# Kernel tuning notes

Measured on AMD Instinct MI355X. Metric: run time of the kernel, lower is better.

Reference implementation:

```python
import jax, jax.numpy as jnp
import numpy as np

N_MOL = 100000   # molecules in batch
N_ATOMS = 40     # atoms per molecule
R = 2            # resonance representations per molecule


def setup_inputs() -> dict:
    key = jax.random.key(0)
    k1, k2, k3 = jax.random.split(key, 3)
    N = N_MOL * N_ATOMS * R  # flattened atom rows (8M)
    electronegativity = jax.random.normal(k1, (N,), dtype=jnp.float32)
    # hardness must be positive / away from zero (it is inverted)
    hardness = jax.random.uniform(k2, (N,), dtype=jnp.float32, minval=0.5, maxval=1.5)
    formal_charge = jax.random.randint(k3, (N,), -1, 2).astype(jnp.float32)
    idx = jnp.arange(N, dtype=jnp.int32)
    # layout: [mol0 rep0 (40 atoms), mol0 rep1 (40 atoms), mol1 rep0, ...]
    rep_seg = idx // N_ATOMS                       # molecule-representation segment id
    mol = idx // (N_ATOMS * R)
    j = idx % N_ATOMS                              # atom index within molecule
    out_idx = mol * N_ATOMS + j                    # output row for mean over reps
    return {
        "electronegativity": electronegativity,
        "hardness": hardness,
        "formal_charge": formal_charge,
        "rep_seg": rep_seg,
        "out_idx": out_idx,
        "num_segments": N_MOL * R,
        "num_out": N_MOL * N_ATOMS,
        "n_reps": R,
    }


def reference(electronegativity, hardness, formal_charge, rep_seg, out_idx,
              num_segments, num_out, n_reps):
    # Charge equalization (Gilson et al.) per molecule-representation segment s:
    #   inv_h_i = 1/h_i
    #   q_i = inv_h_i * ((dot(inv_h, e) + Q_s) / sum(inv_h) - e_i)
    inv_h = 1.0 / hardness
    A = jax.ops.segment_sum(inv_h, rep_seg, num_segments)                      # sum(1/h)
    B = jax.ops.segment_sum(inv_h * electronegativity, rep_seg, num_segments)  # dot(1/h, e)
    Q = jax.ops.segment_sum(formal_charge, rep_seg, num_segments)              # total charge
    lam = (B + Q) / A                                                          # Lagrange multiplier per segment
    q = inv_h * (lam[rep_seg] - electronegativity)                             # per-atom charge per rep
    # mean over the n_reps representations of each molecule (torch .mean(dim=0) + vstack)
    out = jax.ops.segment_sum(q, out_idx, num_out) / n_reps
    return out.reshape(-1, 1)
```

## Files before the change

### kernel.cpp

```cpp
#include <hip/hip_runtime.h>


#define BLOCK 320
#define MPB   16
#define SEGS  (MPB * 2)
#define ATOMS (MPB * 80)

__global__ __launch_bounds__(BLOCK) void cpc_kernel(
    const float* __restrict__ elneg,
    const float* __restrict__ hard,
    const float* __restrict__ fchg,
    float* __restrict__ out,
    int n_mol)
{
    __shared__ float s_inv[ATOMS];
    __shared__ float s_e[ATOMS];
    __shared__ float s_pa[SEGS * 11];
    __shared__ float s_pb[SEGS * 11];
    __shared__ float s_pq[SEGS * 11];
    __shared__ float s_lam[SEGS];

    const int t = threadIdx.x;
    const long long mol_base = (long long)blockIdx.x * MPB;
    const int lm = (int)min((long long)MPB, (long long)n_mol - mol_base);
    const long long atom_base = mol_base * 80;

    if (t < lm * 20) {
        const int a4 = 4 * t;
        float4 h4 = *reinterpret_cast<const float4*>(hard  + atom_base + a4);
        float4 e4 = *reinterpret_cast<const float4*>(elneg + atom_base + a4);
        float4 f4 = *reinterpret_cast<const float4*>(fchg  + atom_base + a4);
        float4 i4;
        i4.x = 1.0f / h4.x; i4.y = 1.0f / h4.y;
        i4.z = 1.0f / h4.z; i4.w = 1.0f / h4.w;
        *reinterpret_cast<float4*>(&s_inv[a4]) = i4;
        *reinterpret_cast<float4*>(&s_e[a4])   = e4;
        const float pa = (i4.x + i4.y) + (i4.z + i4.w);
        const float pb = (i4.x * e4.x + i4.y * e4.y) + (i4.z * e4.z + i4.w * e4.w);
        const float pq = (f4.x + f4.y) + (f4.z + f4.w);
        const int seg  = t / 10;
        const int slot = t % 10;
        s_pa[seg * 11 + slot] = pa;
        s_pb[seg * 11 + slot] = pb;
        s_pq[seg * 11 + slot] = pq;
    }
    __syncthreads();

    if (t < lm * 2) {
        float A = 0.f, B = 0.f, Q = 0.f;
        #pragma unroll
        for (int k = 0; k < 10; ++k) {
            A += s_pa[t * 11 + k];
            B += s_pb[t * 11 + k];
            Q += s_pq[t * 11 + k];
        }
        s_lam[t] = (B + Q) / A;
    }
    __syncthreads();

    if (t < lm * 10) {
        const int m = t / 10;
        const int j = (t % 10) * 4;
        const float lam0 = s_lam[2 * m];
        const float lam1 = s_lam[2 * m + 1];
        const int p0 = m * 80 + j;
        const int p1 = p0 + 40;
        float4 i0 = *reinterpret_cast<const float4*>(&s_inv[p0]);
        float4 e0 = *reinterpret_cast<const float4*>(&s_e[p0]);
        float4 i1 = *reinterpret_cast<const float4*>(&s_inv[p1]);
        float4 e1 = *reinterpret_cast<const float4*>(&s_e[p1]);
        float4 o;
        o.x = 0.5f * (i0.x * (lam0 - e0.x) + i1.x * (lam1 - e1.x));
        o.y = 0.5f * (i0.y * (lam0 - e0.y) + i1.y * (lam1 - e1.y));
        o.z = 0.5f * (i0.z * (lam0 - e0.z) + i1.z * (lam1 - e1.z));
        o.w = 0.5f * (i0.w * (lam0 - e0.w) + i1.w * (lam1 - e1.w));
        *reinterpret_cast<float4*>(out + mol_base * 40 + 4 * t) = o;
    }
}

extern "C" void kernel_launch(void* const* d_in, const int* in_sizes, int n_in,
                              void* d_out, int out_size, void* d_ws, size_t ws_size,
                              hipStream_t stream) {
    const float* elneg = (const float*)d_in[0];
    const float* hard  = (const float*)d_in[1];
    const float* fchg  = (const float*)d_in[2];
    float* out = (float*)d_out;

    const int n_mol = out_size / 40;
    const int grid  = (n_mol + MPB - 1) / MPB;
    cpc_kernel<<<grid, BLOCK, 0, stream>>>(elneg, hard, fchg, out, n_mol);
}
```

Baseline: 22.17 us.

## Keep atom data in registers, double molecules per block, use nontemporal loads

Each thread now loads both representations of its 4-atom slice, keeps the inverse hardness and electronegativity in registers, and reuses them for the final charge, which removes the shared-memory staging arrays and their stores and reloads. Molecules per block rise from 16 to 32 at 320 threads, so every thread is active and the grid halves. Global loads and stores use nontemporal builtins to avoid polluting the cache with streamed data. Each thread now holds more registers, and the loads of the two representations are strided by 40 floats instead of fully contiguous per thread.

```diff
diff --git a/kernel.cpp b/kernel.cpp
--- a/kernel.cpp
+++ b/kernel.cpp
@@ -1,10 +1,11 @@
 #include <hip/hip_runtime.h>
 
 
+typedef float f32x4 __attribute__((ext_vector_type(4)));
+
 #define BLOCK 320
-#define MPB   16
+#define MPB   32
 #define SEGS  (MPB * 2)
-#define ATOMS (MPB * 80)
 
 __global__ __launch_bounds__(BLOCK) void cpc_kernel(
     const float* __restrict__ elneg,
@@ -13,40 +14,49 @@
     float* __restrict__ out,
     int n_mol)
 {
-    __shared__ float s_inv[ATOMS];
-    __shared__ float s_e[ATOMS];
     __shared__ float s_pa[SEGS * 11];
     __shared__ float s_pb[SEGS * 11];
     __shared__ float s_pq[SEGS * 11];
     __shared__ float s_lam[SEGS];
 
     const int t = threadIdx.x;
+    const int m = t / 10;
+    const int s = t - m * 10;
     const long long mol_base = (long long)blockIdx.x * MPB;
-    const int lm = (int)min((long long)MPB, (long long)n_mol - mol_base);
-    const long long atom_base = mol_base * 80;
+    const int lm = min(MPB, (int)(n_mol - mol_base));
+    const bool act = (m < lm);
 
-    if (t < lm * 20) {
-        const int a4 = 4 * t;
-        float4 h4 = *reinterpret_cast<const float4*>(hard  + atom_base + a4);
-        float4 e4 = *reinterpret_cast<const float4*>(elneg + atom_base + a4);
-        float4 f4 = *reinterpret_cast<const float4*>(fchg  + atom_base + a4);
-        float4 i4;
-        i4.x = 1.0f / h4.x; i4.y = 1.0f / h4.y;
-        i4.z = 1.0f / h4.z; i4.w = 1.0f / h4.w;
-        *reinterpret_cast<float4*>(&s_inv[a4]) = i4;
-        *reinterpret_cast<float4*>(&s_e[a4])   = e4;
-        const float pa = (i4.x + i4.y) + (i4.z + i4.w);
-        const float pb = (i4.x * e4.x + i4.y * e4.y) + (i4.z * e4.z + i4.w * e4.w);
-        const float pq = (f4.x + f4.y) + (f4.z + f4.w);
-        const int seg  = t / 10;
-        const int slot = t % 10;
-        s_pa[seg * 11 + slot] = pa;
-        s_pb[seg * 11 + slot] = pb;
-        s_pq[seg * 11 + slot] = pq;
+    const long long g0 = (mol_base + m) * 80 + 4 * s;
+
+    f32x4 h0, e0, f0, h1, e1, f1;
+    h0.x=1;h0.y=1;h0.z=1;h0.w=1; h1=h0;
+    e0.x=0;e0.y=0;e0.z=0;e0.w=0; e1=e0; f0=e0; f1=e0;
+    if (act) {
+        h0 = __builtin_nontemporal_load((const f32x4*)(hard  + g0));
+        h1 = __builtin_nontemporal_load((const f32x4*)(hard  + g0 + 40));
+        e0 = __builtin_nontemporal_load((const f32x4*)(elneg + g0));
+        e1 = __builtin_nontemporal_load((const f32x4*)(elneg + g0 + 40));
+        f0 = __builtin_nontemporal_load((const f32x4*)(fchg  + g0));
+        f1 = __builtin_nontemporal_load((const f32x4*)(fchg  + g0 + 40));
+    }
+
+    f32x4 i0, i1;
+    i0.x = 1.0f / h0.x; i0.y = 1.0f / h0.y; i0.z = 1.0f / h0.z; i0.w = 1.0f / h0.w;
+    i1.x = 1.0f / h1.x; i1.y = 1.0f / h1.y; i1.z = 1.0f / h1.z; i1.w = 1.0f / h1.w;
+
+    if (act) {
+        const int b0 = (2 * m)     * 11 + s;
+        const int b1 = (2 * m + 1) * 11 + s;
+        s_pa[b0] = (i0.x + i0.y) + (i0.z + i0.w);
+        s_pb[b0] = (i0.x * e0.x + i0.y * e0.y) + (i0.z * e0.z + i0.w * e0.w);
+        s_pq[b0] = (f0.x + f0.y) + (f0.z + f0.w);
+        s_pa[b1] = (i1.x + i1.y) + (i1.z + i1.w);
+        s_pb[b1] = (i1.x * e1.x + i1.y * e1.y) + (i1.z * e1.z + i1.w * e1.w);
+        s_pq[b1] = (f1.x + f1.y) + (f1.z + f1.w);
     }
     __syncthreads();
 
-    if (t < lm * 2) {
+    if (t < 2 * lm) {
         float A = 0.f, B = 0.f, Q = 0.f;
         #pragma unroll
         for (int k = 0; k < 10; ++k) {
@@ -58,23 +68,15 @@
     }
     __syncthreads();
 
-    if (t < lm * 10) {
-        const int m = t / 10;
-        const int j = (t % 10) * 4;
+    if (act) {
         const float lam0 = s_lam[2 * m];
         const float lam1 = s_lam[2 * m + 1];
-        const int p0 = m * 80 + j;
-        const int p1 = p0 + 40;
-        float4 i0 = *reinterpret_cast<const float4*>(&s_inv[p0]);
-        float4 e0 = *reinterpret_cast<const float4*>(&s_e[p0]);
-        float4 i1 = *reinterpret_cast<const float4*>(&s_inv[p1]);
-        float4 e1 = *reinterpret_cast<const float4*>(&s_e[p1]);
-        float4 o;
+        f32x4 o;
         o.x = 0.5f * (i0.x * (lam0 - e0.x) + i1.x * (lam1 - e1.x));
         o.y = 0.5f * (i0.y * (lam0 - e0.y) + i1.y * (lam1 - e1.y));
         o.z = 0.5f * (i0.z * (lam0 - e0.z) + i1.z * (lam1 - e1.z));
         o.w = 0.5f * (i0.w * (lam0 - e0.w) + i1.w * (lam1 - e1.w));
-        *reinterpret_cast<float4*>(out + mol_base * 40 + 4 * t) = o;
+        __builtin_nontemporal_store(o, (f32x4*)(out + (mol_base + m) * 40 + 4 * s));
     }
 }
 
```

Result: slower. 23.93 us (+8.0%).
